# Kernel optimization log

Measured on AMD Instinct MI355X. Metric: run time of the kernel, lower is better.

The kernel has to match this reference:

```python
import jax, jax.numpy as jnp
import numpy as np

EMB_DIM = 256
ATT_DIM = 256
B, S = 8, 2048


def setup_inputs() -> dict:
    key = jax.random.key(0)
    ks = jax.random.split(key, 9)
    scale = 1.0 / np.sqrt(EMB_DIM)
    inp = {
        "x": jax.random.normal(ks[0], (B, S, EMB_DIM), dtype=jnp.float32),
        "mask": jax.random.randint(ks[1], (B, S, S), 0, 2, dtype=jnp.int32),
        "Wq": jax.random.uniform(ks[2], (EMB_DIM, ATT_DIM), jnp.float32, -scale, scale),
        "bq": jax.random.uniform(ks[3], (ATT_DIM,), jnp.float32, -scale, scale),
        "Wk": jax.random.uniform(ks[4], (EMB_DIM, ATT_DIM), jnp.float32, -scale, scale),
        "bk": jax.random.uniform(ks[5], (ATT_DIM,), jnp.float32, -scale, scale),
        "Wv": jax.random.uniform(ks[6], (EMB_DIM, ATT_DIM), jnp.float32, -scale, scale),
        "bv": jax.random.uniform(ks[7], (ATT_DIM,), jnp.float32, -scale, scale),
    }
    return inp


def reference(x, mask, Wq, bq, Wk, bk, Wv, bv):
    # Linear projections: (B,S,E) @ (E,A) + (A,)
    q = jnp.einsum("bse,ea->bsa", x, Wq) + bq
    k = jnp.einsum("bse,ea->bsa", x, Wk) + bk
    v = jnp.einsum("bse,ea->bsa", x, Wv) + bv
    # scores: (B,S,S)
    scores = jnp.einsum("bqa,bka->bqk", q, k) / jnp.sqrt(jnp.float32(ATT_DIM))
    scores = jnp.where(mask == 0, jnp.float32(-1e9), scores)
    attn = jax.nn.softmax(scores, axis=-1)
    return jnp.einsum("bqk,bka->bqa", attn, v)
```

## Files before the change

### kernel.cpp

```cpp
#include <hip/hip_runtime.h>
#include <hip/hip_bf16.h>
#include <stdint.h>

#define BATCH 8
#define SEQ   2048
#define EMB   256
#define ADIM  256

typedef __bf16 bf16_t;
typedef __attribute__((ext_vector_type(8))) __bf16 bf16x8;
typedef __attribute__((ext_vector_type(4))) float  f32x4;
typedef uint32_t u32;
typedef long long i64;

static __device__ __forceinline__ f32x4 mfma16(bf16x8 a, bf16x8 b, f32x4 c) {
    return __builtin_amdgcn_mfma_f32_16x16x32_bf16(a, b, c, 0, 0, 0);
}

static __device__ __forceinline__ void gld16(const void* g, void* l) {
    __builtin_amdgcn_global_load_lds((const __attribute__((address_space(1))) u32*)g,
                                     (__attribute__((address_space(3))) u32*)l, 16, 0, 0);
}

__global__ __launch_bounds__(256) void wtkv_kernel(const float* __restrict__ Wk,
                                                   const float* __restrict__ Wv,
                                                   bf16_t* __restrict__ wt) {
    int tid = blockIdx.x * 256 + threadIdx.x;
    int m = tid >> 16;
    int i = tid & 65535;
    int a = i >> 8, e = i & 255;
    const float* W = (m == 0) ? Wk : Wv;
    wt[m * 65536 + a * 256 + e] = (bf16_t)W[e * 256 + a];
}

__global__ __launch_bounds__(128, 1) void proj_kv(const float* __restrict__ x,
                                                  const bf16_t* __restrict__ wt,
                                                  const float* __restrict__ bk,
                                                  const float* __restrict__ bv,
                                                  char* __restrict__ Ksw,
                                                  char* __restrict__ Vsw) {
    __shared__ __align__(16) char stg[2][10240];
    const int tid  = threadIdx.x;
    const int wid  = tid >> 6;
    const int lane = tid & 63;
    const int lq   = lane >> 4;
    const int ln   = lane & 15;
    const int blk  = blockIdx.x;
    const int b    = blk >> 6;
    const int tile = blk & 63;
    const int mbase = blk * 32 + wid * 16;
    char* S = stg[wid];

    bf16x8 xf[8];
    const float* xp = x + (size_t)(mbase + ln) * EMB;
    #pragma unroll
    for (int c = 0; c < 8; ++c) {
        f32x4 a0 = *(const f32x4*)(xp + c * 32 + lq * 8);
        f32x4 a1 = *(const f32x4*)(xp + c * 32 + lq * 8 + 4);
        bf16x8 v;
        v[0] = (bf16_t)a0[0]; v[1] = (bf16_t)a0[1]; v[2] = (bf16_t)a0[2]; v[3] = (bf16_t)a0[3];
        v[4] = (bf16_t)a1[0]; v[5] = (bf16_t)a1[1]; v[6] = (bf16_t)a1[2]; v[7] = (bf16_t)a1[3];
        xf[c] = v;
    }

    f32x4 acc[16];

    #pragma unroll
    for (int t = 0; t < 16; ++t) acc[t] = (f32x4){0.f, 0.f, 0.f, 0.f};
    {
        const bf16_t* w = wt;
        #pragma unroll
        for (int c = 0; c < 8; ++c)
            #pragma unroll
            for (int t = 0; t < 16; ++t) {
                bf16x8 wf = *(const bf16x8*)(w + (size_t)(t * 16 + ln) * 256 + c * 32 + lq * 8);
                acc[t] = mfma16(xf[c], wf, acc[t]);
            }
    }
    #pragma unroll
    for (int t = 0; t < 16; ++t) {
        float bb = bk[t * 16 + ln];
        #pragma unroll
        for (int r = 0; r < 4; ++r)
            *(bf16_t*)(S + (lq * 4 + r) * 512 + (t * 16 + ln) * 2) = (bf16_t)(acc[t][r] + bb);
    }
    asm volatile("s_waitcnt lgkmcnt(0)" ::: "memory");
    {
        char* Kg = Ksw + (size_t)b * 1048576 + (size_t)tile * 16384 + wid * 8192;
        const int rh = lane >> 5;
        const int p  = lane & 31;
        #pragma unroll
        for (int i = 0; i < 8; ++i) {
            int row = i * 2 + rh;
            int n   = wid * 16 + row;
            int cb  = p ^ (n & 7);
            f32x4 ch = *(const f32x4*)(S + row * 512 + cb * 16);
            *(f32x4*)(Kg + row * 512 + p * 16) = ch;
        }
    }

    #pragma unroll
    for (int t = 0; t < 16; ++t) acc[t] = (f32x4){0.f, 0.f, 0.f, 0.f};
    {
        const bf16_t* w = wt + 65536;
        #pragma unroll
        for (int c = 0; c < 8; ++c)
            #pragma unroll
            for (int t = 0; t < 16; ++t) {
                bf16x8 wf = *(const bf16x8*)(w + (size_t)(t * 16 + ln) * 256 + c * 32 + lq * 8);
                acc[t] = mfma16(xf[c], wf, acc[t]);
            }
    }
    #pragma unroll
    for (int t = 0; t < 16; ++t) {
        float bb = bv[t * 16 + ln];
        #pragma unroll
        for (int r = 0; r < 4; ++r)
            *(bf16_t*)(S + (t * 16 + ln) * 40 + (lq * 4 + r) * 2) = (bf16_t)(acc[t][r] + bb);
    }
    asm volatile("s_waitcnt lgkmcnt(0)" ::: "memory");
    {
        char* Vg = Vsw + (size_t)b * 1048576 + (size_t)tile * 16384;
        const int half = lane & 1;
        const int kq   = wid * 2 + half;
        #pragma unroll
        for (int i = 0; i < 8; ++i) {
            int a   = i * 32 + (lane >> 1);
            int pos = kq ^ (a & 3) ^ ((a >> 2) & 3);
            f32x4 ch = *(const f32x4*)(S + a * 40 + half * 16);
            *(f32x4*)(Vg + a * 64 + pos * 16) = ch;
        }
    }
}

__global__ __launch_bounds__(256, 2) void flash_kernel(const float* __restrict__ x,
                                                       const float* __restrict__ WqM,
                                                       const float* __restrict__ bq,
                                                       const char* __restrict__ Ksw,
                                                       const char* __restrict__ Vsw,
                                                       const int* __restrict__ mask,
                                                       float* __restrict__ lp,
                                                       i64 bs, i64 rs, i64 ks,
                                                       float* __restrict__ out) {
    __shared__ __align__(16) char smem[71168];
    const int tid  = threadIdx.x;
    const int wid  = tid >> 6;
    const int lane = tid & 63;
    const int lq   = lane >> 4;
    const int ln   = lane & 15;
    const int qw   = wid >> 1;
    const int kw   = wid & 1;
    const int batch = blockIdx.x & 7;
    const int kvh   = (blockIdx.x >> 3) & 1;
    const int qbase = (blockIdx.x >> 4) * 64;

    const char* Kb = Ksw + (size_t)batch * 1048576 + (size_t)(kvh * 32) * 16384;
    const char* Vb = Vsw + (size_t)batch * 1048576 + (size_t)(kvh * 32) * 16384;
    char*  Pq_ = smem + 65536 + qw * 2560;
    char*  Pt  = smem + 65536 + wid * 1280;
    float* Ls  = (float*)(smem + 70656);

    const char* kg0 = Kb + wid * 4096 + lane * 16;
    const char* vg0 = Vb + wid * 4096 + lane * 16;

    const int* mroot = mask + (size_t)batch * SEQ * SEQ +
                       (size_t)(qbase + qw * 32) * SEQ + kvh * 1024 + kw * 16 + ln;

    {
        char* kl = smem + wid * 4096;
        char* vl = smem + 16384 + wid * 4096;
        #pragma unroll
        for (int i = 0; i < 4; ++i) gld16(kg0 + i * 1024, kl + i * 1024);
        #pragma unroll
        for (int i = 0; i < 4; ++i) gld16(vg0 + i * 1024, vl + i * 1024);
    }
    int mv[2][2][4];
    #pragma unroll
    for (int w = 0; w < 2; ++w)
        #pragma unroll
        for (int h = 0; h < 2; ++h)
            #pragma unroll
            for (int r = 0; r < 4; ++r)
                mv[w][h][r] = mroot[(size_t)(h * 16 + lq * 4 + r) * SEQ + w * 32];

    bf16x8 qf[2][8];
    {
        bf16x8 xf[2][8];
        #pragma unroll
        for (int h = 0; h < 2; ++h) {
            const float* xp = x + (size_t)(batch * SEQ + qbase + qw * 32 + h * 16 + ln) * EMB;
            #pragma unroll
            for (int c = 0; c < 8; ++c) {
                f32x4 a = *(const f32x4*)(xp + c * 32 + lq * 8);
                f32x4 b = *(const f32x4*)(xp + c * 32 + lq * 8 + 4);
                bf16x8 v;
                v[0] = (bf16_t)a[0]; v[1] = (bf16_t)a[1]; v[2] = (bf16_t)a[2]; v[3] = (bf16_t)a[3];
                v[4] = (bf16_t)b[0]; v[5] = (bf16_t)b[1]; v[6] = (bf16_t)b[2]; v[7] = (bf16_t)b[3];
                xf[h][c] = v;
            }
        }
        f32x4 qacc[2][16];
        #pragma unroll
        for (int h = 0; h < 2; ++h)
            #pragma unroll
            for (int t = 0; t < 16; ++t) qacc[h][t] = (f32x4){0.f, 0.f, 0.f, 0.f};

        char* Wsp = smem + 32768;
        const int e = ln & 7;
        #pragma unroll 1
        for (int cp = 0; cp < 8; ++cp) {
            __syncthreads();
            const float* wqp = WqM + (size_t)(cp * 32) * 256 + tid;
            #pragma unroll
            for (int i = 0; i < 4; ++i) {
                bf16x8 pk;
                #pragma unroll
                for (int j = 0; j < 8; ++j)
                    pk[j] = (bf16_t)wqp[(size_t)(i * 8 + j) * 256];
                *(bf16x8*)(Wsp + tid * 128 + ((i ^ (tid & 7)) * 16)) = pk;
            }
            __syncthreads();
            #pragma unroll
            for (int t = 0; t < 16; ++t) {
                bf16x8 wf = *(const bf16x8*)(Wsp + (t * 16 + ln) * 128 + ((lq ^ e) * 16));
                qacc[0][t] = mfma16(xf[0][cp], wf, qacc[0][t]);
                qacc[1][t] = mfma16(xf[1][cp], wf, qacc[1][t]);
            }
        }
        #pragma unroll
        for (int h = 0; h < 2; ++h) {
            #pragma unroll
            for (int c = 0; c < 8; ++c) {
                #pragma unroll
                for (int half2 = 0; half2 < 2; ++half2) {
                    int t = 2 * c + half2;
                    float bb = bq[t * 16 + ln];
                    #pragma unroll
                    for (int r = 0; r < 4; ++r) {
                        float v = (qacc[h][t][r] + bb) * 0.0625f;
                        ((bf16_t*)(Pt + (lq * 4 + r) * 80))[half2 * 16 + ln] = (bf16_t)v;
                    }
                }
                qf[h][c] = *(const bf16x8*)(Pt + ln * 80 + lq * 16);
            }
        }
    }

    f32x4 o[2][8];
    #pragma unroll
    for (int h = 0; h < 2; ++h)
        #pragma unroll
        for (int t = 0; t < 8; ++t) o[h][t] = (f32x4){0.f, 0.f, 0.f, 0.f};
    float lsum[2][4] = {{0.f,0.f,0.f,0.f},{0.f,0.f,0.f,0.f}};

    const int kswz = ln & 7;
    const int vswz = (lq ^ (ln & 3) ^ ((ln >> 2) & 3)) * 16;
    const int n0   = kw * 16 + ln;

    for (int kt = 0; kt < 32; ++kt) {
        __syncthreads();
        if (kt + 1 < 32) {
            int nb = (kt + 1) & 1;
            const char* kg = kg0 + (size_t)(kt + 1) * 16384;
            const char* vg = vg0 + (size_t)(kt + 1) * 16384;
            char* kl = smem + nb * 32768 + wid * 4096;
            char* vl = smem + nb * 32768 + 16384 + wid * 4096;
            #pragma unroll
            for (int i = 0; i < 4; ++i) gld16(kg + i * 1024, kl + i * 1024);
            #pragma unroll
            for (int i = 0; i < 4; ++i) gld16(vg + i * 1024, vl + i * 1024);
        }
        const int buf = kt & 1;
        const char* Ksb = smem + buf * 32768;
        const char* Vsb = smem + buf * 32768 + 16384;

        f32x4 s0 = (f32x4){0.f,0.f,0.f,0.f};
        f32x4 s1 = (f32x4){0.f,0.f,0.f,0.f};
        const char* krow = Ksb + n0 * 512;
        __builtin_amdgcn_s_setprio(1);
        #pragma unroll
        for (int c = 0; c < 8; ++c) {
            bf16x8 kf = *(const bf16x8*)(krow + (((c * 4 + lq) ^ kswz) * 16));
            s0 = mfma16(qf[0][c], kf, s0);
            s1 = mfma16(qf[1][c], kf, s1);
        }
        __builtin_amdgcn_s_setprio(0);

        const int (*mc)[4] = mv[kt & 1];
        #pragma unroll
        for (int r = 0; r < 4; ++r) {
            float p0 = mc[0][r] ? __expf(s0[r]) : 0.f;
            float p1 = mc[1][r] ? __expf(s1[r]) : 0.f;
            lsum[0][r] += p0;
            lsum[1][r] += p1;
            ((bf16_t*)(Pq_ + (lq * 4 + r) * 80))[kw * 16 + ln]      = (bf16_t)p0;
            ((bf16_t*)(Pq_ + (16 + lq * 4 + r) * 80))[kw * 16 + ln] = (bf16_t)p1;
        }

        {
            const int ktn = (kt + 2 < 32) ? kt + 2 : 31;
            int (*md)[4] = mv[kt & 1];
            #pragma unroll
            for (int h = 0; h < 2; ++h)
                #pragma unroll
                for (int r = 0; r < 4; ++r)
                    md[h][r] = mroot[(size_t)(h * 16 + lq * 4 + r) * SEQ + ktn * 32];
        }

        asm volatile("s_waitcnt lgkmcnt(0)\n\ts_barrier" ::: "memory");

        bf16x8 pa0 = *(const bf16x8*)(Pq_ + ln * 80 + lq * 16);
        bf16x8 pa1 = *(const bf16x8*)(Pq_ + (16 + ln) * 80 + lq * 16);

        const char* vbase = Vsb + (kw * 128 + ln) * 64 + vswz;
        __builtin_amdgcn_s_setprio(1);
        #pragma unroll
        for (int t = 0; t < 8; ++t) {
            bf16x8 vf = *(const bf16x8*)(vbase + t * 1024);
            o[0][t] = mfma16(pa0, vf, o[0][t]);
            o[1][t] = mfma16(pa1, vf, o[1][t]);
        }
        __builtin_amdgcn_s_setprio(0);
    }

    __syncthreads();
    #pragma unroll
    for (int h = 0; h < 2; ++h) {
        #pragma unroll
        for (int r = 0; r < 4; ++r) {
            float v = lsum[h][r];
            v += __shfl_xor(v, 1);
            v += __shfl_xor(v, 2);
            v += __shfl_xor(v, 4);
            v += __shfl_xor(v, 8);
            if (ln == 0) Ls[(qw * 2 + kw) * 32 + h * 16 + lq * 4 + r] = v;
            lsum[h][r] = v;
        }
    }
    __syncthreads();

    if (kw == 0 && ln == 0) {
        #pragma unroll
        for (int h = 0; h < 2; ++h)
            #pragma unroll
            for (int r = 0; r < 4; ++r) {
                int row = h * 16 + lq * 4 + r;
                float tot = lsum[h][r] + Ls[(qw * 2 + 1) * 32 + row];
                lp[bs * batch + rs * (qbase + qw * 32 + row) + ks * kvh] = tot;
            }
    }

    #pragma unroll
    for (int h = 0; h < 2; ++h) {
        #pragma unroll
        for (int r = 0; r < 4; ++r) {
            float* orow = out + (size_t)(batch * SEQ + qbase + qw * 32 + h * 16 + lq * 4 + r) * ADIM
                          + kw * 128 + ln;
            #pragma unroll
            for (int t = 0; t < 8; ++t)
                atomicAdd(orow + t * 16, o[h][t][r]);
        }
    }
}

__global__ __launch_bounds__(256) void merge_kernel(const float* __restrict__ lp,
                                                    i64 bs, i64 rs, i64 ks,
                                                    float* __restrict__ out) {
    int idx  = blockIdx.x * 256 + threadIdx.x;
    int base = idx * 4;
    int row  = base >> 8;
    int b = row >> 11, r = row & 2047;
    float l0 = lp[bs * b + rs * r];
    float l1 = lp[bs * b + rs * r + ks];
    float inv = 1.0f / (l0 + l1);
    f32x4 v = *(const f32x4*)(out + base);
    v[0] *= inv; v[1] *= inv; v[2] *= inv; v[3] *= inv;
    *(f32x4*)(out + base) = v;
}

extern "C" void kernel_launch(void* const* d_in, const int* in_sizes, int n_in,
                              void* d_out, int out_size, void* d_ws, size_t ws_size,
                              hipStream_t stream) {
    const float* x    = (const float*)d_in[0];
    int*         mask = (int*)d_in[1];
    const float* Wq   = (const float*)d_in[2];
    const float* bq   = (const float*)d_in[3];
    const float* Wk   = (const float*)d_in[4];
    const float* bk   = (const float*)d_in[5];
    const float* Wv   = (const float*)d_in[6];
    const float* bv   = (const float*)d_in[7];
    float* out = (float*)d_out;

    char* Ksw = (char*)d_ws;
    char* Vsw = Ksw + (size_t)8 * 1024 * 1024;
    bf16_t* wt = (bf16_t*)d_out;

    const size_t need = (size_t)16 * 1024 * 1024 + (size_t)2 * BATCH * SEQ * sizeof(float);
    float* lp; i64 bs, rs, ks;
    if (ws_size >= need) {
        lp = (float*)(Ksw + (size_t)16 * 1024 * 1024);
        bs = (i64)2 * SEQ;  rs = 2;  ks = 1;
    } else {
        lp = (float*)mask;
        bs = (i64)SEQ * SEQ;  rs = SEQ;  ks = 1024;
    }

    wtkv_kernel<<<512, 256, 0, stream>>>(Wk, Wv, wt);
    proj_kv<<<512, 128, 0, stream>>>(x, wt, bk, bv, Ksw, Vsw);
    hipMemsetAsync(d_out, 0, (size_t)out_size * sizeof(float), stream);
    flash_kernel<<<512, 256, 0, stream>>>(x, Wq, bq, Ksw, Vsw, mask, lp, bs, rs, ks, out);
    merge_kernel<<<4096, 256, 0, stream>>>(lp, bs, rs, ks, out);
}
```

Before: 378.5 us.

## Pack int32 mask into bitwords and relax flash loop barriers

Adds a pre-pass kernel that compresses the int32 mask into 32-bit bitmasks in workspace, so the flash kernel reads mask bits instead of full int32 values per key. The flash loop also replaces __syncthreads with a partial vmcnt wait plus barrier, moves the mask prefetch after the P barrier, and drops the s_setprio hints. The mask still has to be read once in full by the pre-pass, so total mask traffic is not reduced; the gain depends on the flash kernel's scattered mask loads costing more than a streaming pass. The path is used only when the workspace is large enough.

```diff
diff --git a/kernel.cpp b/kernel.cpp
--- a/kernel.cpp
+++ b/kernel.cpp
@@ -11,6 +11,7 @@
 typedef __attribute__((ext_vector_type(8))) __bf16 bf16x8;
 typedef __attribute__((ext_vector_type(4))) float  f32x4;
 typedef uint32_t u32;
+typedef __attribute__((ext_vector_type(4))) u32 u32x4;
 typedef long long i64;
 
 static __device__ __forceinline__ f32x4 mfma16(bf16x8 a, bf16x8 b, f32x4 c) {
@@ -31,6 +32,21 @@
     int a = i >> 8, e = i & 255;
     const float* W = (m == 0) ? Wk : Wv;
     wt[m * 65536 + a * 256 + e] = (bf16_t)W[e * 256 + a];
+}
+
+__global__ __launch_bounds__(256) void maskbits_kernel(const u32* __restrict__ mask,
+                                                       u32* __restrict__ bitw) {
+    int idx = blockIdx.x * 256 + threadIdx.x;
+    const u32* mp = mask + (size_t)idx * 32;
+    u32 wd = 0;
+    #pragma unroll
+    for (int q = 0; q < 8; ++q) {
+        u32x4 v = *(const u32x4*)(mp + q * 4);
+        #pragma unroll
+        for (int j = 0; j < 4; ++j)
+            wd |= (v[j] ? 1u : 0u) << (q * 4 + j);
+    }
+    bitw[idx] = wd;
 }
 
 __global__ __launch_bounds__(128, 1) void proj_kv(const float* __restrict__ x,
@@ -139,6 +155,7 @@
                                                        const char* __restrict__ Ksw,
                                                        const char* __restrict__ Vsw,
                                                        const int* __restrict__ mask,
+                                                       const u32* __restrict__ bitw,
                                                        float* __restrict__ lp,
                                                        i64 bs, i64 rs, i64 ks,
                                                        float* __restrict__ out) {
@@ -165,6 +182,10 @@
 
     const int* mroot = mask + (size_t)batch * SEQ * SEQ +
                        (size_t)(qbase + qw * 32) * SEQ + kvh * 1024 + kw * 16 + ln;
+    const u32* broot = bitw ? bitw + (size_t)batch * 131072 +
+                              (size_t)(qbase + qw * 32) * 64 + kvh * 32
+                            : nullptr;
+    const int bitpos = kw * 16 + ln;
 
     {
         char* kl = smem + wid * 4096;
@@ -174,14 +195,25 @@
         #pragma unroll
         for (int i = 0; i < 4; ++i) gld16(vg0 + i * 1024, vl + i * 1024);
     }
+    asm volatile("" ::: "memory");
     int mv[2][2][4];
-    #pragma unroll
-    for (int w = 0; w < 2; ++w)
-        #pragma unroll
-        for (int h = 0; h < 2; ++h)
-            #pragma unroll
-            for (int r = 0; r < 4; ++r)
-                mv[w][h][r] = mroot[(size_t)(h * 16 + lq * 4 + r) * SEQ + w * 32];
+    if (broot) {
+        #pragma unroll
+        for (int w = 0; w < 2; ++w)
+            #pragma unroll
+            for (int h = 0; h < 2; ++h)
+                #pragma unroll
+                for (int r = 0; r < 4; ++r)
+                    mv[w][h][r] = (int)((broot[(h * 16 + lq * 4 + r) * 64 + w] >> bitpos) & 1u);
+    } else {
+        #pragma unroll
+        for (int w = 0; w < 2; ++w)
+            #pragma unroll
+            for (int h = 0; h < 2; ++h)
+                #pragma unroll
+                for (int r = 0; r < 4; ++r)
+                    mv[w][h][r] = mroot[(size_t)(h * 16 + lq * 4 + r) * SEQ + w * 32];
+    }
 
     bf16x8 qf[2][8];
     {
@@ -258,7 +290,7 @@
     const int n0   = kw * 16 + ln;
 
     for (int kt = 0; kt < 32; ++kt) {
-        __syncthreads();
+        asm volatile("s_waitcnt vmcnt(8) lgkmcnt(0)\n\ts_barrier" ::: "memory");
         if (kt + 1 < 32) {
             int nb = (kt + 1) & 1;
             const char* kg = kg0 + (size_t)(kt + 1) * 16384;
@@ -277,14 +309,12 @@
         f32x4 s0 = (f32x4){0.f,0.f,0.f,0.f};
         f32x4 s1 = (f32x4){0.f,0.f,0.f,0.f};
         const char* krow = Ksb + n0 * 512;
-        __builtin_amdgcn_s_setprio(1);
         #pragma unroll
         for (int c = 0; c < 8; ++c) {
             bf16x8 kf = *(const bf16x8*)(krow + (((c * 4 + lq) ^ kswz) * 16));
             s0 = mfma16(qf[0][c], kf, s0);
             s1 = mfma16(qf[1][c], kf, s1);
         }
-        __builtin_amdgcn_s_setprio(0);
 
         const int (*mc)[4] = mv[kt & 1];
         #pragma unroll
@@ -297,30 +327,36 @@
             ((bf16_t*)(Pq_ + (16 + lq * 4 + r) * 80))[kw * 16 + ln] = (bf16_t)p1;
         }
 
+        asm volatile("s_waitcnt lgkmcnt(0)\n\ts_barrier" ::: "memory");
+
         {
             const int ktn = (kt + 2 < 32) ? kt + 2 : 31;
             int (*md)[4] = mv[kt & 1];
-            #pragma unroll
-            for (int h = 0; h < 2; ++h)
-                #pragma unroll
-                for (int r = 0; r < 4; ++r)
-                    md[h][r] = mroot[(size_t)(h * 16 + lq * 4 + r) * SEQ + ktn * 32];
-        }
-
-        asm volatile("s_waitcnt lgkmcnt(0)\n\ts_barrier" ::: "memory");
+            if (broot) {
+                #pragma unroll
+                for (int h = 0; h < 2; ++h)
+                    #pragma unroll
+                    for (int r = 0; r < 4; ++r)
+                        md[h][r] = (int)((broot[(h * 16 + lq * 4 + r) * 64 + ktn] >> bitpos) & 1u);
+            } else {
+                #pragma unroll
+                for (int h = 0; h < 2; ++h)
+                    #pragma unroll
+                    for (int r = 0; r < 4; ++r)
+                        md[h][r] = mroot[(size_t)(h * 16 + lq * 4 + r) * SEQ + ktn * 32];
+            }
+        }
 
         bf16x8 pa0 = *(const bf16x8*)(Pq_ + ln * 80 + lq * 16);
         bf16x8 pa1 = *(const bf16x8*)(Pq_ + (16 + ln) * 80 + lq * 16);
 
         const char* vbase = Vsb + (kw * 128 + ln) * 64 + vswz;
-        __builtin_amdgcn_s_setprio(1);
         #pragma unroll
         for (int t = 0; t < 8; ++t) {
             bf16x8 vf = *(const bf16x8*)(vbase + t * 1024);
             o[0][t] = mfma16(pa0, vf, o[0][t]);
             o[1][t] = mfma16(pa1, vf, o[1][t]);
         }
-        __builtin_amdgcn_s_setprio(0);
     }
 
     __syncthreads();
@@ -395,10 +431,16 @@
     char* Vsw = Ksw + (size_t)8 * 1024 * 1024;
     bf16_t* wt = (bf16_t*)d_out;
 
-    const size_t need = (size_t)16 * 1024 * 1024 + (size_t)2 * BATCH * SEQ * sizeof(float);
+    const size_t MB = 1024 * 1024;
+    const size_t lsum_bytes = (size_t)2 * BATCH * SEQ * sizeof(float);
+    u32*   bitw = nullptr;
     float* lp; i64 bs, rs, ks;
-    if (ws_size >= need) {
-        lp = (float*)(Ksw + (size_t)16 * 1024 * 1024);
+    if (ws_size >= 20 * MB + lsum_bytes) {
+        bitw = (u32*)(Ksw + 16 * MB);
+        lp = (float*)(Ksw + 20 * MB);
+        bs = (i64)2 * SEQ;  rs = 2;  ks = 1;
+    } else if (ws_size >= 16 * MB + lsum_bytes) {
+        lp = (float*)(Ksw + 16 * MB);
         bs = (i64)2 * SEQ;  rs = 2;  ks = 1;
     } else {
         lp = (float*)mask;
@@ -406,8 +448,10 @@
     }
 
     wtkv_kernel<<<512, 256, 0, stream>>>(Wk, Wv, wt);
+    if (bitw) maskbits_kernel<<<4096, 256, 0, stream>>>((const u32*)mask, bitw);
     proj_kv<<<512, 128, 0, stream>>>(x, wt, bk, bv, Ksw, Vsw);
     hipMemsetAsync(d_out, 0, (size_t)out_size * sizeof(float), stream);
-    flash_kernel<<<512, 256, 0, stream>>>(x, Wq, bq, Ksw, Vsw, mask, lp, bs, rs, ks, out);
+    flash_kernel<<<512, 256, 0, stream>>>(x, Wq, bq, Ksw, Vsw, mask, bitw,
+                                          lp, bs, rs, ks, out);
     merge_kernel<<<4096, 256, 0, stream>>>(lp, bs, rs, ks, out);
 }
```

After: 367.1 us. 3.0% less time.
